# Kernel optimization log

Hardware: AMD Instinct MI355X
Metric: run time of the kernel (lower is better)

The kernel has to match this reference:

```python
import jax, jax.numpy as jnp
import numpy as np

B, T, IN, H, OUT = 64, 32, 256, 512, 256
M, W, R = 256, 64, 4            # nr_cells, cell_size, read_heads
NN_IN = IN + R * W              # 512
NN_OUT = H + R * W              # 768
IFACE = R * W + 3 * W + 5 * R + 3  # 471
CLIP = 20.0
DELTA = 1e-6


def setup_inputs():
    key = jax.random.key(0)
    ks = jax.random.split(key, 10)
    s = 0.05
    bound = float(np.sqrt(6.0 / (B * H + 2 * H)))  # xavier_uniform on (2,B,H)
    return {
        'x': jax.random.normal(ks[0], (B, T, IN), jnp.float32),
        'h0': jax.random.uniform(ks[1], (2, B, H), jnp.float32, -bound, bound),
        'Wih0': jax.random.normal(ks[2], (4 * H, NN_IN), jnp.float32) * s,
        'Whh0': jax.random.normal(ks[3], (4 * H, H), jnp.float32) * s,
        'bih0': jnp.zeros((4 * H,), jnp.float32),
        'bhh0': jnp.zeros((4 * H,), jnp.float32),
        'Wih1': jax.random.normal(ks[4], (4 * H, H), jnp.float32) * s,
        'Whh1': jax.random.normal(ks[5], (4 * H, H), jnp.float32) * s,
        'bih1': jnp.zeros((4 * H,), jnp.float32),
        'bhh1': jnp.zeros((4 * H,), jnp.float32),
        'Wif': jax.random.normal(ks[6], (IFACE, H), jnp.float32) * s,
        'bif': jnp.zeros((IFACE,), jnp.float32),
        'Wout': jax.random.normal(ks[7], (OUT, NN_OUT), jnp.float32) * s,
        'bout': jnp.zeros((OUT,), jnp.float32),
    }


def _lstm_cell(x, h, c, Wih, Whh, bih, bhh):
    g = x @ Wih.T + bih + h @ Whh.T + bhh
    i, f, gg, o = jnp.split(g, 4, axis=1)  # torch gate order i,f,g,o
    c = jax.nn.sigmoid(f) * c + jax.nn.sigmoid(i) * jnp.tanh(gg)
    h = jax.nn.sigmoid(o) * jnp.tanh(c)
    return h, c


def _content_weights(mem, keys, strengths):
    # mem: (b,M,W), keys: (b,K,W), strengths: (b,K) -> softmax over M
    mem_n = mem / (jnp.linalg.norm(mem, axis=2, keepdims=True) + DELTA)
    key_n = keys / (jnp.linalg.norm(keys, axis=2, keepdims=True) + DELTA)
    sim = jnp.einsum('bkw,bmw->bkm', key_n, mem_n)
    return jax.nn.softmax(sim * strengths[..., None], axis=2)


def _memory_step(xi, mem, link, prec, rw, ww, usage):
    b = xi.shape[0]
    o = 0
    rk = jnp.tanh(xi[:, :R * W].reshape(b, R, W)); o = R * W
    rs = jax.nn.softplus(xi[:, o:o + R]); o += R
    wk = jnp.tanh(xi[:, o:o + W]).reshape(b, 1, W); o += W
    ws = jax.nn.softplus(xi[:, o])[:, None]; o += 1
    ev = jax.nn.sigmoid(xi[:, o:o + W]); o += W
    wv = jnp.tanh(xi[:, o:o + W]); o += W
    fg = jax.nn.sigmoid(xi[:, o:o + R]); o += R
    ag = jax.nn.sigmoid(xi[:, o])[:, None]; o += 1
    wg = jax.nn.sigmoid(xi[:, o])[:, None]; o += 1
    rm = jax.nn.softmax(xi[:, o:o + 3 * R].reshape(b, R, 3), axis=2)

    # usage update (uses OLD read/write weights); single write head
    usage = usage + (1.0 - usage) * ww
    psi = jnp.prod(1.0 - fg[:, :, None] * rw, axis=1)
    usage = usage * psi

    # write content addressing on OLD memory
    wcw = _content_weights(mem, wk, ws)[:, 0]  # (b,M)

    # allocation by ascending sort of usage (exclusive cumprod)
    u = DELTA + (1.0 - DELTA) * usage
    phi = jnp.argsort(u, axis=1)
    sorted_u = jnp.take_along_axis(u, phi, axis=1)
    excl = jnp.cumprod(jnp.concatenate([jnp.ones((b, 1), u.dtype), sorted_u], axis=1), axis=1)[:, :-1]
    sorted_alloc = (1.0 - sorted_u) * excl
    alloc = jnp.take_along_axis(sorted_alloc, jnp.argsort(phi, axis=1), axis=1)

    ww = wg * (ag * alloc + (1.0 - ag) * wcw)  # (b,M)

    # erase + write
    mem = mem * (1.0 - ww[:, :, None] * ev[:, None, :]) + ww[:, :, None] * wv[:, None, :]

    # temporal link matrix + precedence
    prev_scale = 1.0 - ww[:, :, None] - ww[:, None, :]
    link = prev_scale * link + ww[:, :, None] * prec[:, None, :]
    link = link * (1.0 - jnp.eye(M, dtype=link.dtype))
    prec = (1.0 - ww.sum(axis=1, keepdims=True)) * prec + ww

    # read: directional weights use NEW link and OLD read weights; content uses NEW memory
    rcw = _content_weights(mem, rk, rs)               # (b,R,M)
    fwd = jnp.einsum('bij,brj->bri', link, rw)
    bwd = jnp.einsum('brj,bji->bri', rw, link)
    rw = rm[:, :, 0:1] * bwd + rm[:, :, 1:2] * fwd + rm[:, :, 2:3] * rcw
    rvec = jnp.einsum('brm,bmw->brw', rw, mem).reshape(b, R * W)
    return rvec, mem, link, prec, rw, ww, usage


def reference(x, h0, Wih0, Whh0, bih0, bhh0, Wih1, Whh1, bih1, bhh1, Wif, bif, Wout, bout):
    b = x.shape[0]
    lr0 = jnp.zeros((b, R * W), x.dtype)  # initial last_read; NOTE: source concatenates this
    # initial zero last_read to EVERY timestep's controller input (inputs built upfront)
    carry0 = (h0[0], h0[0], h0[1], h0[1],
              jnp.full((b, M, W), DELTA, x.dtype),   # memory
              jnp.zeros((b, M, M), x.dtype),          # link matrix
              jnp.zeros((b, M), x.dtype),             # precedence
              jnp.full((b, R, M), DELTA, x.dtype),    # read weights
              jnp.full((b, M), DELTA, x.dtype),       # write weights
              jnp.zeros((b, M), x.dtype))             # usage

    def step(carry, x_t):
        h0_, c0_, h1_, c1_, mem, link, prec, rw, ww, usage = carry
        inp = jnp.concatenate([x_t, lr0], axis=1)
        h0_, c0_ = _lstm_cell(inp, h0_, c0_, Wih0, Whh0, bih0, bhh0)
        h1_, c1_ = _lstm_cell(h0_, h1_, c1_, Wih1, Whh1, bih1, bhh1)
        out = jnp.clip(h1_, -CLIP, CLIP)
        xi = out @ Wif.T + bif
        rvec, mem, link, prec, rw, ww, usage = _memory_step(xi, mem, link, prec, rw, ww, usage)
        o_t = jnp.concatenate([out, rvec], axis=1)  # (b, NN_OUT)
        return (h0_, c0_, h1_, c1_, mem, link, prec, rw, ww, usage), o_t

    _, ys = jax.lax.scan(step, carry0, jnp.swapaxes(x, 0, 1))  # (T,b,NN_OUT)
    outputs = jnp.tanh(ys) @ Wout.T + bout  # Dropout(p=0) -> Tanh -> Linear
    return jnp.swapaxes(outputs, 0, 1)      # (b,T,OUT)
```

## Files before the change

### kernel.cpp

```cpp
#include <hip/hip_runtime.h>
#include <hip/hip_bf16.h>
#include <math.h>


typedef __bf16 bf16_t;
typedef __attribute__((ext_vector_type(8))) __bf16 bf16x8;
typedef __attribute__((ext_vector_type(4))) float f32x4;

#define B_    64
#define T_    32
#define IN_   256
#define H_    512
#define M_    256
#define W_    64
#define R_    4
#define IFACE_ 471
#define DELTA_ 1e-6f

#define OFF_H0SEQ  (0L)
#define SZ_H0SEQ   (32L*64*512*2)
#define OFF_OUTSEQ (OFF_H0SEQ + SZ_H0SEQ)
#define SZ_OUTSEQ  (32L*64*512*2)
#define OFF_H0BUF  (OFF_OUTSEQ + SZ_OUTSEQ)
#define SZ_HBUF    (2L*64*512*2)
#define OFF_H1BUF  (OFF_H0BUF + SZ_HBUF)
#define OFF_XI     (OFF_H1BUF + SZ_HBUF)
#define SZ_XI      (32L*64*480*4)
#define OFF_RVEC   (OFF_XI + SZ_XI)
#define SZ_RVEC    (32L*64*256*4)
#define OFF_YBF    (OFF_RVEC + SZ_RVEC)
#define SZ_YBF     (32L*64*768*2)
#define OFF_BAR    (OFF_YBF + SZ_YBF)
#define SZ_BAR     (256L)
#define OFF_XB     (OFF_BAR + SZ_BAR)
#define SZ_XB      (64L*32*256*2)
#define OFF_H0B    (OFF_XB + SZ_XB)
#define SZ_H0B     (2L*64*512*2)
#define OFF_W0     (OFF_H0B + SZ_H0B)
#define SZ_W       (2048L*512*2)
#define OFF_W1     (OFF_W0 + SZ_W)
#define OFF_W2     (OFF_W1 + SZ_W)
#define OFF_W3     (OFF_W2 + SZ_W)
#define OFF_WIF    (OFF_W3 + SZ_W)
#define SZ_WIF     (480L*512*2)
#define OFF_WOUTB  (OFF_WIF + SZ_WIF)
#define SZ_WOUTB   (256L*768*2)
#define OFF_BS0    (OFF_WOUTB + SZ_WOUTB)
#define SZ_BS      (2048L*4)
#define OFF_BS1    (OFF_BS0 + SZ_BS)
#define OFF_BIF    (OFF_BS1 + SZ_BS)
#define SZ_BIF     (2048L)
#define OFF_BOUTF  (OFF_BIF + SZ_BIF)
#define SZ_BOUTF   (1024L)
#define OFF_FLG    (OFF_BOUTF + SZ_BOUTF)
#define SZ_FLG     (4096L)

__device__ __forceinline__ float frcp(float x){ return __builtin_amdgcn_rcpf(x); }
__device__ __forceinline__ float fsqrt_(float x){ return __builtin_amdgcn_sqrtf(x); }
__device__ __forceinline__ float sigf(float x){ return frcp(1.0f + __expf(-x)); }
__device__ __forceinline__ float tanh_f(float x){
  float xc = fminf(fmaxf(x, -44.0f), 44.0f);
  float t = __expf(2.0f * xc);
  return (t - 1.0f) * frcp(t + 1.0f);
}
__device__ __forceinline__ float softplusf(float x){
  return fmaxf(x, 0.0f) + __logf(1.0f + __expf(-fabsf(x)));
}
__device__ __forceinline__ float wred(float v){
  #pragma unroll
  for (int off = 32; off; off >>= 1) v += __shfl_xor(v, off, 64);
  return v;
}
__device__ __forceinline__ float ldin(const void* p, long i, int mf){
  return mf ? ((const float*)p)[i] : (float)((const bf16_t*)p)[i];
}

__device__ __forceinline__ unsigned flag_ld(const unsigned* p){
  return __hip_atomic_load(p, __ATOMIC_RELAXED, __HIP_MEMORY_SCOPE_AGENT);
}

__device__ __forceinline__ void flagbar(unsigned* flg, int bid, unsigned tgt,
                                        int tid, int lane, int wv){
  __syncthreads();
  if (tid == 0)
    __hip_atomic_store(flg + (size_t)bid*16, tgt, __ATOMIC_RELEASE,
                       __HIP_MEMORY_SCOPE_AGENT);
  if (wv == 0){
    for (;;){
      unsigned f = flag_ld(flg + (size_t)lane*16);
      if (__all(f >= tgt)) break;
      __builtin_amdgcn_s_sleep(2);
    }
    __builtin_amdgcn_fence(__ATOMIC_ACQUIRE, "agent");
  }
  __syncthreads();
}

__global__ void k_detect(const unsigned short* __restrict__ x16,
                         int* __restrict__ flag, unsigned* __restrict__ bar,
                         unsigned* __restrict__ flg){
  __shared__ int cnt;
  if (threadIdx.x == 0){ cnt = 0; bar[0] = 0u; bar[1] = 0u; }
  for (int i = threadIdx.x; i < 1024; i += 256) flg[i] = 0u;
  __syncthreads();
  unsigned short u = x16[threadIdx.x * 2];
  int e = (u >> 7) & 0xFF;
  if (e >= 0x88) atomicAdd(&cnt, 1);
  __syncthreads();
  if (threadIdx.x == 0) *flag = (cnt > 16) ? 1 : 0;
}

__global__ void k_convert(const void* x, const void* h0, const void* Wih0,
                          const void* Whh0, const void* bih0, const void* bhh0,
                          const void* Wih1, const void* Whh1, const void* bih1,
                          const void* bhh1, const void* Wif, const void* bif,
                          const void* Wout, const void* bout,
                          bf16_t* __restrict__ xb, bf16_t* __restrict__ h0b,
                          bf16_t* __restrict__ h0buf, bf16_t* __restrict__ h1buf,
                          bf16_t* __restrict__ W0, bf16_t* __restrict__ W1,
                          bf16_t* __restrict__ W2, bf16_t* __restrict__ W3,
                          bf16_t* __restrict__ Wifp, bf16_t* __restrict__ Woutb,
                          float* __restrict__ bs0, float* __restrict__ bs1,
                          float* __restrict__ bifp, float* __restrict__ boutf,
                          const int* __restrict__ flag)
{
  const int mf = *flag;
  const long stride = (long)gridDim.x * blockDim.x;
  long i0 = (long)blockIdx.x * blockDim.x + threadIdx.x;
  switch (blockIdx.y){
  case 0: for (long i = i0; i < 64L*32*256; i += stride) xb[i] = (bf16_t)ldin(x, i, mf); break;
  case 1: for (long i = i0; i < 2L*64*512; i += stride){
            float v = ldin(h0, i, mf); bf16_t bb = (bf16_t)v; h0b[i] = bb;
            if (i < 64*512) h0buf[i] = bb; else h1buf[i - 64*512] = bb;
          } break;
  case 2: for (long i = i0; i < 2048L*512; i += stride) W0[i] = (bf16_t)ldin(Wih0, i, mf); break;
  case 3: for (long i = i0; i < 2048L*512; i += stride) W1[i] = (bf16_t)ldin(Whh0, i, mf); break;
  case 4: for (long i = i0; i < 2048L*512; i += stride) W2[i] = (bf16_t)ldin(Wih1, i, mf); break;
  case 5: for (long i = i0; i < 2048L*512; i += stride) W3[i] = (bf16_t)ldin(Whh1, i, mf); break;
  case 6: for (long i = i0; i < 480L*512; i += stride){
            long r = i >> 9;
            Wifp[i] = (r < IFACE_) ? (bf16_t)ldin(Wif, i, mf) : (bf16_t)0.0f;
          } break;
  case 7: for (long i = i0; i < 256L*768; i += stride) Woutb[i] = (bf16_t)ldin(Wout, i, mf); break;
  case 8:
    for (long i = i0; i < 2048; i += stride){
      bs0[i] = ldin(bih0, i, mf) + ldin(bhh0, i, mf);
      bs1[i] = ldin(bih1, i, mf) + ldin(bhh1, i, mf);
    }
    for (long i = i0; i < 480; i += stride) bifp[i] = (i < IFACE_) ? ldin(bif, i, mf) : 0.0f;
    for (long i = i0; i < 256; i += stride) boutf[i] = ldin(bout, i, mf);
    break;
  }
}

__device__ __forceinline__ void softmax256_wave(float* a, int lane){
  float v0=a[lane], v1=a[64+lane], v2=a[128+lane], v3=a[192+lane];
  float mx = fmaxf(fmaxf(v0,v1), fmaxf(v2,v3));
  #pragma unroll
  for (int off=32; off; off>>=1) mx = fmaxf(mx, __shfl_xor(mx, off, 64));
  v0=__expf(v0-mx); v1=__expf(v1-mx); v2=__expf(v2-mx); v3=__expf(v3-mx);
  float s = v0+v1+v2+v3;
  #pragma unroll
  for (int off=32; off; off>>=1) s += __shfl_xor(s, off, 64);
  float inv = frcp(s);
  a[lane]=v0*inv; a[64+lane]=v1*inv; a[128+lane]=v2*inv; a[192+lane]=v3*inv;
}

struct ProdShm {
  bf16_t wpool[66560];
  float  cst[64][16];
  float  bias[4][16];
};
struct ConsShm {
  float smem[256][65];
  float xib[480];
  float rkn4r[2][65][4];
  float wkn[64], ev_[64], wvv[64];
  float rs_[4], fg_[4], rm_[4][3];
  float wsS, agS, wgS, wwsumS;
  float invn[256], wcw[256];
  float usage[256], uu[256], su[256], scanA[256];
  int   rank_[256];
  float ww_[256], prec_[256];
  float rw_[4][256];
  float rw4[256][4];
  float fwd_[4][256], bwd_[4][256], rcw_[4][256];
  bf16_t rwb[4][264];
  bf16_t wwb[256], precb[256];
  float p2cT[2][264];
  float p5cT[5][2][264];
  float rvp[8][4][64];
};
union ShUnion { ProdShm p; ConsShm c; };

__global__ __launch_bounds__(512) void k_main(
    const bf16_t* __restrict__ xb, const bf16_t* __restrict__ h0b,
    const bf16_t* __restrict__ W0, const bf16_t* __restrict__ W1,
    const bf16_t* __restrict__ W2, const bf16_t* __restrict__ W3,
    const float* __restrict__ bs0, const float* __restrict__ bs1,
    const bf16_t* __restrict__ Wifp, const float* __restrict__ bifp,
    bf16_t* __restrict__ h0buf, bf16_t* __restrict__ h1buf,
    bf16_t* __restrict__ h0seq, bf16_t* __restrict__ outseq,
    float* __restrict__ XI, float* __restrict__ RVEC,
    unsigned* __restrict__ flg)
{
  __shared__ ShUnion sh;
  const int bid = blockIdx.x;
  const int tid = threadIdx.x, lane = tid & 63, wv = tid >> 6;
  const int m16 = lane & 15, q = lane >> 4;

  if (bid < 64){
    ProdShm& P = sh.p;
    const int layer = bid >> 5;
    const int u0 = (bid & 31) * 16;

    if (!layer){
      for (int i = tid; i < 64*32; i += 512){
        int rl = i >> 5, c8 = (i & 31)*8;
        int grow = (rl >> 4)*512 + u0 + (rl & 15);
        *(bf16x8*)&P.wpool[rl*264 + c8] = *(const bf16x8*)(W0 + (size_t)grow*512 + c8);
      }
      for (int i = tid; i < 64*64; i += 512){
        int rl = i >> 6, c8 = (i & 63)*8;
        int grow = (rl >> 4)*512 + u0 + (rl & 15);
        *(bf16x8*)&P.wpool[16896 + rl*520 + c8] = *(const bf16x8*)(W1 + (size_t)grow*512 + c8);
      }
    } else {
      for (int i = tid; i < 64*64; i += 512){
        int rl = i >> 6, c8 = (i & 63)*8;
        int grow = (rl >> 4)*512 + u0 + (rl & 15);
        *(bf16x8*)&P.wpool[rl*520 + c8]         = *(const bf16x8*)(W2 + (size_t)grow*512 + c8);
        *(bf16x8*)&P.wpool[33280 + rl*520 + c8] = *(const bf16x8*)(W3 + (size_t)grow*512 + c8);
      }
    }
    for (int i = tid; i < 64*16; i += 512){
      int b = i >> 4, n = i & 15;
      P.cst[b][n] = (float)h0b[layer*(64*512) + b*512 + u0 + n];
    }
    if (tid < 64){
      int G = tid >> 4, n = tid & 15;
      const float* bs = layer ? bs1 : bs0;
      P.bias[G][n] = bs[G*512 + u0 + n];
    }
    __syncthreads();

    bf16_t* hbuf = layer ? h1buf : h0buf;

    for (int ps = 0; ps <= 33; ++ps){
      if (wv < 4){
        const int t = layer ? (ps - 1) : ps;
        const bool active = layer ? (ps >= 1 && ps <= 32) : (ps < 32);
        if (active){
          const int p = t & 1;
          const bf16_t* hin = hbuf + p*(64*512);
          bf16_t* hout = hbuf + (p^1)*(64*512);
          const int b0 = wv * 16;

          f32x4 acc[4];
          #pragma unroll
          for (int G = 0; G < 4; ++G){ float bv = P.bias[G][m16]; acc[G] = (f32x4){bv,bv,bv,bv}; }

          if (!layer){
            #pragma unroll 2
            for (int kt = 0; kt < 8; ++kt){
              bf16x8 a = *(const bf16x8*)(xb + ((size_t)(b0+m16)*T_ + t)*IN_ + kt*32 + q*8);
              #pragma unroll
              for (int G = 0; G < 4; ++G)
                acc[G] = __builtin_amdgcn_mfma_f32_16x16x32_bf16(
                    a, *(const bf16x8*)&P.wpool[(G*16+m16)*264 + kt*32 + q*8], acc[G], 0, 0, 0);
            }
            #pragma unroll 4
            for (int kt = 0; kt < 16; ++kt){
              bf16x8 a = *(const bf16x8*)(hin + (b0+m16)*512 + kt*32 + q*8);
              #pragma unroll
              for (int G = 0; G < 4; ++G)
                acc[G] = __builtin_amdgcn_mfma_f32_16x16x32_bf16(
                    a, *(const bf16x8*)&P.wpool[16896 + (G*16+m16)*520 + kt*32 + q*8], acc[G], 0, 0, 0);
            }
          } else {
            #pragma unroll 4
            for (int kt = 0; kt < 16; ++kt){
              bf16x8 a = *(const bf16x8*)(h0seq + ((size_t)t*64 + b0+m16)*512 + kt*32 + q*8);
              #pragma unroll
              for (int G = 0; G < 4; ++G)
                acc[G] = __builtin_amdgcn_mfma_f32_16x16x32_bf16(
                    a, *(const bf16x8*)&P.wpool[(G*16+m16)*520 + kt*32 + q*8], acc[G], 0, 0, 0);
            }
            #pragma unroll 4
            for (int kt = 0; kt < 16; ++kt){
              bf16x8 a = *(const bf16x8*)(hin + (b0+m16)*512 + kt*32 + q*8);
              #pragma unroll
              for (int G = 0; G < 4; ++G)
                acc[G] = __builtin_amdgcn_mfma_f32_16x16x32_bf16(
                    a, *(const bf16x8*)&P.wpool[33280 + (G*16+m16)*520 + kt*32 + q*8], acc[G], 0, 0, 0);
            }
          }
          #pragma unroll
          for (int v = 0; v < 4; ++v){
            int b = b0 + q*4 + v;
            float gi = acc[0][v], gf = acc[1][v], gg = acc[2][v], go = acc[3][v];
            float c_ = sigf(gf)*P.cst[b][m16] + sigf(gi)*tanh_f(gg);
            P.cst[b][m16] = c_;
            float h = sigf(go)*tanh_f(c_);
            bf16_t hb = (bf16_t)h;
            hout[b*512 + u0 + m16] = hb;
            if (!layer) h0seq[((size_t)t*64 + b)*512 + u0 + m16] = hb;
            else        outseq[((size_t)t*64 + b)*512 + u0 + m16] = hb;
          }
        }
      } else if (ps >= 2 && bid < 30){
        const int t2 = ps - 2;
        const int b0 = (wv - 4) * 16;
        const int r = bid*16 + m16;
        float bv = bifp[r];
        f32x4 acc = {bv,bv,bv,bv};
        const bf16_t* arow = outseq + ((size_t)t2*64 + b0 + m16)*512 + q*8;
        const bf16_t* brow = Wifp + (size_t)r*512 + q*8;
        #pragma unroll 4
        for (int kt = 0; kt < 16; ++kt){
          acc = __builtin_amdgcn_mfma_f32_16x16x32_bf16(
              *(const bf16x8*)(arow + kt*32), *(const bf16x8*)(brow + kt*32), acc, 0, 0, 0);
        }
        #pragma unroll
        for (int v = 0; v < 4; ++v)
          XI[((size_t)t2*64 + b0 + q*4 + v)*480 + r] = acc[v];
      }
      flagbar(flg, bid, (unsigned)(ps + 1), tid, lane, wv);
    }
  } else {
    ConsShm& S = sh.c;
    const int b = bid - 64;
    const int quad = lane >> 4, li = lane & 15;

    bf16x8 rowL[2][8], colL[2][8];
    #pragma unroll
    for (int g = 0; g < 2; ++g)
      #pragma unroll
      for (int ch = 0; ch < 8; ++ch)
        #pragma unroll
        for (int z = 0; z < 8; ++z){ rowL[g][ch][z] = (bf16_t)0.0f; colL[g][ch][z] = (bf16_t)0.0f; }

    float mr[32];
    #pragma unroll
    for (int z = 0; z < 32; ++z) mr[z] = DELTA_;

    if (tid < 256){
      S.ww_[tid] = DELTA_; S.usage[tid] = 0.0f; S.prec_[tid] = 0.0f;
      S.invn[tid] = 1.0f/(fsqrt_(64.0f*DELTA_*DELTA_) + DELTA_);
      S.wwb[tid] = (bf16_t)DELTA_; S.precb[tid] = (bf16_t)0.0f;
      #pragma unroll
      for (int r = 0; r < 4; ++r) S.rw_[r][tid] = DELTA_;
    }
    for (int i = tid; i < 4*264; i += 512) ((bf16_t*)S.rwb)[i] = (bf16_t)DELTA_;
    for (int i = tid; i < 256*65; i += 512) ((float*)S.smem)[i] = DELTA_;
    __syncthreads();

    const int mH = tid >> 1, q2 = tid & 1;

    for (int t = 0; t < 32; ++t){
      { const unsigned tgt = (unsigned)(t + 3);
        if (wv == 0){
          for (;;){
            unsigned f = flag_ld(flg + (size_t)lane*16);
            if (__all(f >= tgt)) break;
            __builtin_amdgcn_s_sleep(2);
          }
          __builtin_amdgcn_fence(__ATOMIC_ACQUIRE, "agent");
        }
        __syncthreads();
      }
      if (tid < IFACE_) S.xib[tid] = XI[((size_t)t*64 + b)*480 + tid];
      __syncthreads();

      if (wv < 4){
        float v = tanh_f(S.xib[wv*64 + lane]);
        float s = wred(v*v);
        float vn = v * frcp(fsqrt_(s) + DELTA_);
        S.rkn4r[0][lane][wv] = vn; S.rkn4r[1][lane][wv] = vn;
      } else if (wv == 4){
        float v = tanh_f(S.xib[260 + lane]);
        float s = wred(v*v);
        S.wkn[lane] = v * frcp(fsqrt_(s) + DELTA_);
      } else if (wv == 5){ S.ev_[lane] = sigf(S.xib[325 + lane]);
      } else if (wv == 6){ S.wvv[lane] = tanh_f(S.xib[389 + lane]);
      } else {
        if (lane < 4)        S.rs_[lane] = softplusf(S.xib[256 + lane]);
        else if (lane == 4)  S.wsS = softplusf(S.xib[324]);
        else if (lane < 9)   S.fg_[lane-5] = sigf(S.xib[453 + (lane-5)]);
        else if (lane == 9)  S.agS = sigf(S.xib[457]);
        else if (lane == 10) S.wgS = sigf(S.xib[458]);
        else if (lane >= 16 && lane < 20){
          int r = lane - 16;
          float a0 = S.xib[459+r*3], a1 = S.xib[459+r*3+1], a2 = S.xib[459+r*3+2];
          float mx = fmaxf(a0, fmaxf(a1, a2));
          float e0 = __expf(a0-mx), e1 = __expf(a1-mx), e2 = __expf(a2-mx);
          float inv = frcp(e0+e1+e2);
          S.rm_[r][0]=e0*inv; S.rm_[r][1]=e1*inv; S.rm_[r][2]=e2*inv;
        }
      }
      __syncthreads();

      if (tid < 256){
        int m = tid;
        float us = S.usage[m] + (1.0f - S.usage[m])*S.ww_[m];
        float psi = (1.0f - S.fg_[0]*S.rw_[0][m]) * (1.0f - S.fg_[1]*S.rw_[1][m])
                  * (1.0f - S.fg_[2]*S.rw_[2][m]) * (1.0f - S.fg_[3]*S.rw_[3][m]);
        us *= psi;
        S.usage[m] = us;
        S.uu[m] = DELTA_ + (1.0f - DELTA_)*us;
      }
      { float acc = 0.0f;
        #pragma unroll
        for (int it = 0; it < 32; ++it){
          int w = q2*32 + it;
          acc += mr[it] * S.wkn[w];
        }
        S.p2cT[q2][mH] = acc; }
      __syncthreads();

      if (wv == 0){
        #pragma unroll
        for (int z = 0; z < 4; ++z){
          int m = z*64 + lane;
          S.wcw[m] = S.wsS * (S.p2cT[0][m] + S.p2cT[1][m]) * S.invn[m];
        }
        softmax256_wave(S.wcw, lane);
      } else if (tid >= 256){
        const int i = tid - 256;
        const float ui = S.uu[i];
        int cnt = 0;
        #pragma unroll 8
        for (int k = 0; k < 64; ++k){
          f32x4 u4 = *(const f32x4*)&S.uu[k*4];
          #pragma unroll
          for (int z = 0; z < 4; ++z){
            int j = k*4 + z; float uj = u4[z];
            cnt += (uj < ui || (uj == ui && j < i)) ? 1 : 0;
          }
        }
        S.rank_[i] = cnt;
        S.su[cnt] = ui;
      }
      __syncthreads();

      if (wv == 0){
        int base = lane*4;
        float v0 = S.su[base], v1 = S.su[base+1], v2 = S.su[base+2];
        float p1 = v0*v1, p2 = p1*v2, p3 = p2*S.su[base+3];
        float sc = p3;
        #pragma unroll
        for (int off = 1; off < 64; off <<= 1){
          float n = __shfl_up(sc, off, 64);
          if (lane >= off) sc *= n;
        }
        float exch = __shfl_up(sc, 1, 64);
        if (lane == 0) exch = 1.0f;
        S.scanA[base] = exch; S.scanA[base+1] = exch*v0;
        S.scanA[base+2] = exch*p1; S.scanA[base+3] = exch*p2;
      }
      __syncthreads();

      { const int m = mH;
        float al = (1.0f - S.uu[m]) * S.scanA[S.rank_[m]];
        float wm = S.wgS*(S.agS*al + (1.0f - S.agS)*S.wcw[m]);
        if (q2 == 0){ S.ww_[m] = wm; S.wwb[m] = (bf16_t)wm; }
        float s2 = 0.0f, sr0 = 0.0f, sr1 = 0.0f, sr2 = 0.0f, sr3 = 0.0f;
        #pragma unroll
        for (int it = 0; it < 32; ++it){
          int w = q2*32 + it;
          float mn = mr[it]*(1.0f - wm*S.ev_[w]) + wm*S.wvv[w];
          mr[it] = mn;
          S.smem[m][w] = mn;
          s2 += mn*mn;
          f32x4 rk = *(const f32x4*)&S.rkn4r[q2][w][0];
          sr0 += mn*rk[0]; sr1 += mn*rk[1]; sr2 += mn*rk[2]; sr3 += mn*rk[3];
        }
        S.p5cT[0][q2][m] = s2;
        S.p5cT[1][q2][m] = sr0; S.p5cT[2][q2][m] = sr1;
        S.p5cT[3][q2][m] = sr2; S.p5cT[4][q2][m] = sr3; }
      __syncthreads();

      if (tid < 256){
        int m = tid;
        float s2 = S.p5cT[0][0][m] + S.p5cT[0][1][m];
        float inv = frcp(fsqrt_(s2) + DELTA_);
        S.invn[m] = inv;
        #pragma unroll
        for (int r = 0; r < 4; ++r){
          float sr = S.p5cT[r+1][0][m] + S.p5cT[r+1][1][m];
          S.rcw_[r][m] = S.rs_[r]*sr*inv;
        }
      } else if (wv == 4){
        float s = wred(S.ww_[lane] + S.ww_[64+lane] + S.ww_[128+lane] + S.ww_[192+lane]);
        if (lane == 0) S.wwsumS = s;
      }
      __syncthreads();

      { float wown[2], pown[2], alpha[2];
        #pragma unroll
        for (int g = 0; g < 2; ++g){
          int o = wv*32 + g*16 + li;
          wown[g] = (float)S.wwb[o]; pown[g] = (float)S.precb[o];
          alpha[g] = 1.0f - wown[g];
        }
        f32x4 facc[2] = {{0,0,0,0},{0,0,0,0}}, bacc[2] = {{0,0,0,0},{0,0,0,0}};
        #pragma unroll
        for (int ch = 0; ch < 8; ++ch){
          const int cbase = ch*32 + quad*8;
          bf16x8 rwf = *(const bf16x8*)&S.rwb[li & 3][cbase];
          bf16x8 wwv = *(const bf16x8*)&S.wwb[cbase];
          bf16x8 pcv = *(const bf16x8*)&S.precb[cbase];
          float wcf[8], pcf[8];
          #pragma unroll
          for (int jj = 0; jj < 8; ++jj){ wcf[jj] = (float)wwv[jj]; pcf[jj] = (float)pcv[jj]; }
          #pragma unroll
          for (int g = 0; g < 2; ++g){
            const int o = wv*32 + g*16 + li;
            bf16x8 rl = rowL[g][ch];
            bf16x8 cl = colL[g][ch];
            #pragma unroll
            for (int jj = 0; jj < 8; ++jj){
              const int c = cbase + jj;
              float s = alpha[g] - wcf[jj];
              float vr = s*(float)rl[jj] + wown[g]*pcf[jj];
              float vc = s*(float)cl[jj] + wcf[jj]*pown[g];
              if (c == o){ vr = 0.0f; vc = 0.0f; }
              rl[jj] = (bf16_t)vr;
              cl[jj] = (bf16_t)vc;
            }
            rowL[g][ch] = rl; colL[g][ch] = cl;
            facc[g] = __builtin_amdgcn_mfma_f32_16x16x32_bf16(rl, rwf, facc[g], 0, 0, 0);
            bacc[g] = __builtin_amdgcn_mfma_f32_16x16x32_bf16(rwf, cl, bacc[g], 0, 0, 0);
          }
        }
        #pragma unroll
        for (int g = 0; g < 2; ++g){
          if (li < 4){
            #pragma unroll
            for (int z = 0; z < 4; ++z) S.fwd_[li][wv*32 + g*16 + quad*4 + z] = facc[g][z];
          }
          if (quad == 0){
            #pragma unroll
            for (int z = 0; z < 4; ++z) S.bwd_[z][wv*32 + g*16 + li] = bacc[g][z];
          }
        }
      }
      __syncthreads();

      if (wv < 4) softmax256_wave(S.rcw_[wv], lane);
      else {
        int m = tid - 256;
        float p = (1.0f - S.wwsumS)*S.prec_[m] + S.ww_[m];
        S.prec_[m] = p;
        S.precb[m] = (bf16_t)p;
      }
      __syncthreads();

      { int r = tid >> 7, m0 = (tid & 127)*2;
        #pragma unroll
        for (int z = 0; z < 2; ++z){
          int m = m0 + z;
          float v = S.rm_[r][0]*S.bwd_[r][m] + S.rm_[r][1]*S.fwd_[r][m] + S.rm_[r][2]*S.rcw_[r][m];
          S.rw_[r][m] = v;
          S.rw4[m][r] = v;
          S.rwb[r][m] = (bf16_t)v;
        } }
      __syncthreads();

      { float r0 = 0, r1 = 0, r2 = 0, r3 = 0;
        #pragma unroll
        for (int k = 0; k < 32; ++k){
          int m = wv*32 + k;
          f32x4 r4 = *(const f32x4*)&S.rw4[m][0];
          float mv = S.smem[m][lane];
          r0 += r4[0]*mv; r1 += r4[1]*mv; r2 += r4[2]*mv; r3 += r4[3]*mv;
        }
        S.rvp[wv][0][lane] = r0; S.rvp[wv][1][lane] = r1;
        S.rvp[wv][2][lane] = r2; S.rvp[wv][3][lane] = r3; }
      __syncthreads();

      if (tid < 256){
        const int w = tid & 63, r = tid >> 6;
        float v = 0.0f;
        #pragma unroll
        for (int c = 0; c < 8; ++c) v += S.rvp[c][r][w];
        RVEC[((size_t)t*64 + b)*256 + tid] = v;
      }
      __syncthreads();
    }
  }
}

__global__ void k_tanhy(const bf16_t* __restrict__ outseq, const float* __restrict__ RVEC,
                        bf16_t* __restrict__ Y){
  const int n = 2048*768;
  for (int i = blockIdx.x*blockDim.x + threadIdx.x; i < n; i += gridDim.x*blockDim.x){
    int row = i / 768, j = i - row*768;
    float v = (j < 512) ? (float)outseq[(size_t)row*512 + j] : RVEC[(size_t)row*256 + (j - 512)];
    Y[i] = (bf16_t)tanh_f(v);
  }
}

__global__ __launch_bounds__(256,1) void k_out(
    const bf16_t* __restrict__ Y, const bf16_t* __restrict__ Woutb,
    const float* __restrict__ boutf, void* __restrict__ dout,
    const int* __restrict__ flag)
{
  const int mf = *flag;
  const int mt = blockIdx.x;
  const int tid = threadIdx.x, lane = tid & 63, wv = tid >> 6;
  const int nt = blockIdx.y*4 + wv;
  const int m16 = lane & 15, q = lane >> 4;
  const int o = nt*16 + m16;
  float bv = boutf[o];
  f32x4 acc = {bv,bv,bv,bv};
  const bf16_t* arow = Y + (size_t)(mt*16 + m16)*768 + q*8;
  const bf16_t* brow = Woutb + (size_t)o*768 + q*8;
  for (int kt = 0; kt < 24; ++kt){
    acc = __builtin_amdgcn_mfma_f32_16x16x32_bf16(
        *(const bf16x8*)(arow + kt*32), *(const bf16x8*)(brow + kt*32), acc, 0, 0, 0);
  }
  #pragma unroll
  for (int v = 0; v < 4; ++v){
    int row = mt*16 + q*4 + v;
    int b = row & 63, t = row >> 6;
    size_t idx = ((size_t)b*T_ + t)*256 + o;
    if (mf) ((float*)dout)[idx] = acc[v];
    else    ((bf16_t*)dout)[idx] = (bf16_t)acc[v];
  }
}

extern "C" void kernel_launch(void* const* d_in, const int* in_sizes, int n_in,
                              void* d_out, int out_size, void* d_ws, size_t ws_size,
                              hipStream_t stream)
{
  char* ws = (char*)d_ws;
  bf16_t* H0SEQ  = (bf16_t*)(ws + OFF_H0SEQ);
  bf16_t* OUTSEQ = (bf16_t*)(ws + OFF_OUTSEQ);
  bf16_t* H0BUF  = (bf16_t*)(ws + OFF_H0BUF);
  bf16_t* H1BUF  = (bf16_t*)(ws + OFF_H1BUF);
  float*  XI     = (float*) (ws + OFF_XI);
  float*  RVEC   = (float*) (ws + OFF_RVEC);
  bf16_t* YBF    = (bf16_t*)(ws + OFF_YBF);
  unsigned* BAR  = (unsigned*)(ws + OFF_BAR);
  int*    FLAG   = (int*)   (ws + OFF_BAR + 8);
  bf16_t* XB     = (bf16_t*)(ws + OFF_XB);
  bf16_t* H0B    = (bf16_t*)(ws + OFF_H0B);
  bf16_t* W0     = (bf16_t*)(ws + OFF_W0);
  bf16_t* W1     = (bf16_t*)(ws + OFF_W1);
  bf16_t* W2     = (bf16_t*)(ws + OFF_W2);
  bf16_t* W3     = (bf16_t*)(ws + OFF_W3);
  bf16_t* WIFP   = (bf16_t*)(ws + OFF_WIF);
  bf16_t* WOUTB  = (bf16_t*)(ws + OFF_WOUTB);
  float*  BS0    = (float*) (ws + OFF_BS0);
  float*  BS1    = (float*) (ws + OFF_BS1);
  float*  BIFP   = (float*) (ws + OFF_BIF);
  float*  BOUTF  = (float*) (ws + OFF_BOUTF);
  unsigned* FLG  = (unsigned*)(ws + OFF_FLG);

  k_detect<<<1, 256, 0, stream>>>((const unsigned short*)d_in[0], FLAG, BAR, FLG);
  k_convert<<<dim3(256, 9), 256, 0, stream>>>(
      d_in[0], d_in[1], d_in[2], d_in[3], d_in[4], d_in[5], d_in[6],
      d_in[7], d_in[8], d_in[9], d_in[10], d_in[11], d_in[12], d_in[13],
      XB, H0B, H0BUF, H1BUF, W0, W1, W2, W3, WIFP, WOUTB,
      BS0, BS1, BIFP, BOUTF, FLAG);
  k_main<<<128, 512, 0, stream>>>(XB, H0B, W0, W1, W2, W3, BS0, BS1,
                                  WIFP, BIFP, H0BUF, H1BUF, H0SEQ, OUTSEQ,
                                  XI, RVEC, FLG);
  k_tanhy<<<512, 256, 0, stream>>>(OUTSEQ, RVEC, YBF);
  k_out<<<dim3(128, 4), 256, 0, stream>>>(YBF, WOUTB, BOUTF, d_out, FLAG);
}
```

Baseline: 1.057 ms.

## Prefetch interface vector into registers and overlap next-step flag wait

The consumer blocks now read their slice of the interface vector straight from global memory into registers instead of staging it through shared memory. The load for the next timestep is issued early, and one wave waits on the producer flag for that step during the precedence update. The bf16 shadow copies of the write weights and precedence are dropped, so the link update reads the fp32 arrays directly. The read-vector reduction is restructured as a two-thread-per-output dot product with a shuffle, replacing the partial-sum buffer and its reduction. Together these remove several barriers per step and take the flag-wait latency off the critical path. The costs are a longer serial loop per thread in the read reduction and more register pressure.

```diff
diff --git a/kernel.cpp b/kernel.cpp
--- a/kernel.cpp
+++ b/kernel.cpp
@@ -173,7 +173,6 @@
 };
 struct ConsShm {
   float smem[256][65];
-  float xib[480];
   float rkn4r[2][65][4];
   float wkn[64], ev_[64], wvv[64];
   float rs_[4], fg_[4], rm_[4][3];
@@ -186,10 +185,8 @@
   float rw4[256][4];
   float fwd_[4][256], bwd_[4][256], rcw_[4][256];
   bf16_t rwb[4][264];
-  bf16_t wwb[256], precb[256];
   float p2cT[2][264];
   float p5cT[5][2][264];
-  float rvp[8][4][64];
 };
 union ShUnion { ProdShm p; ConsShm c; };
 
@@ -344,10 +341,25 @@
     #pragma unroll
     for (int z = 0; z < 32; ++z) mr[z] = DELTA_;
 
+    int off0 = -1, off1 = -1, off2 = -1;
+    if (wv < 4)            off0 = wv*64 + lane;
+    else if (wv == 4)      off0 = 260 + lane;
+    else if (wv == 5)      off0 = 325 + lane;
+    else if (wv == 6)      off0 = 389 + lane;
+    else {
+      if (lane < 4)        off0 = 256 + lane;
+      else if (lane == 4)  off0 = 324;
+      else if (lane < 9)   off0 = 453 + (lane - 5);
+      else if (lane == 9)  off0 = 457;
+      else if (lane == 10) off0 = 458;
+      else if (lane >= 16 && lane < 20){
+        off0 = 459 + (lane - 16)*3; off1 = off0 + 1; off2 = off0 + 2;
+      }
+    }
+
     if (tid < 256){
       S.ww_[tid] = DELTA_; S.usage[tid] = 0.0f; S.prec_[tid] = 0.0f;
       S.invn[tid] = 1.0f/(fsqrt_(64.0f*DELTA_*DELTA_) + DELTA_);
-      S.wwb[tid] = (bf16_t)DELTA_; S.precb[tid] = (bf16_t)0.0f;
       #pragma unroll
       for (int r = 0; r < 4; ++r) S.rw_[r][tid] = DELTA_;
     }
@@ -357,43 +369,44 @@
 
     const int mH = tid >> 1, q2 = tid & 1;
 
+    if (wv == 0){
+      for (;;){
+        unsigned f = flag_ld(flg + (size_t)lane*16);
+        if (__all(f >= 3u)) break;
+        __builtin_amdgcn_s_sleep(2);
+      }
+      __builtin_amdgcn_fence(__ATOMIC_ACQUIRE, "agent");
+    }
+    __syncthreads();
+    float x0 = 0.0f, x1 = 0.0f, x2 = 0.0f;
+    {
+      const float* xp = XI + (size_t)b*480;
+      if (off0 >= 0) x0 = xp[off0];
+      if (off1 >= 0){ x1 = xp[off1]; x2 = xp[off2]; }
+    }
+
     for (int t = 0; t < 32; ++t){
-      { const unsigned tgt = (unsigned)(t + 3);
-        if (wv == 0){
-          for (;;){
-            unsigned f = flag_ld(flg + (size_t)lane*16);
-            if (__all(f >= tgt)) break;
-            __builtin_amdgcn_s_sleep(2);
-          }
-          __builtin_amdgcn_fence(__ATOMIC_ACQUIRE, "agent");
-        }
-        __syncthreads();
-      }
-      if (tid < IFACE_) S.xib[tid] = XI[((size_t)t*64 + b)*480 + tid];
-      __syncthreads();
-
       if (wv < 4){
-        float v = tanh_f(S.xib[wv*64 + lane]);
+        float v = tanh_f(x0);
         float s = wred(v*v);
         float vn = v * frcp(fsqrt_(s) + DELTA_);
         S.rkn4r[0][lane][wv] = vn; S.rkn4r[1][lane][wv] = vn;
       } else if (wv == 4){
-        float v = tanh_f(S.xib[260 + lane]);
+        float v = tanh_f(x0);
         float s = wred(v*v);
         S.wkn[lane] = v * frcp(fsqrt_(s) + DELTA_);
-      } else if (wv == 5){ S.ev_[lane] = sigf(S.xib[325 + lane]);
-      } else if (wv == 6){ S.wvv[lane] = tanh_f(S.xib[389 + lane]);
+      } else if (wv == 5){ S.ev_[lane] = sigf(x0);
+      } else if (wv == 6){ S.wvv[lane] = tanh_f(x0);
       } else {
-        if (lane < 4)        S.rs_[lane] = softplusf(S.xib[256 + lane]);
-        else if (lane == 4)  S.wsS = softplusf(S.xib[324]);
-        else if (lane < 9)   S.fg_[lane-5] = sigf(S.xib[453 + (lane-5)]);
-        else if (lane == 9)  S.agS = sigf(S.xib[457]);
-        else if (lane == 10) S.wgS = sigf(S.xib[458]);
+        if (lane < 4)        S.rs_[lane] = softplusf(x0);
+        else if (lane == 4)  S.wsS = softplusf(x0);
+        else if (lane < 9)   S.fg_[lane-5] = sigf(x0);
+        else if (lane == 9)  S.agS = sigf(x0);
+        else if (lane == 10) S.wgS = sigf(x0);
         else if (lane >= 16 && lane < 20){
           int r = lane - 16;
-          float a0 = S.xib[459+r*3], a1 = S.xib[459+r*3+1], a2 = S.xib[459+r*3+2];
-          float mx = fmaxf(a0, fmaxf(a1, a2));
-          float e0 = __expf(a0-mx), e1 = __expf(a1-mx), e2 = __expf(a2-mx);
+          float mx = fmaxf(x0, fmaxf(x1, x2));
+          float e0 = __expf(x0-mx), e1 = __expf(x1-mx), e2 = __expf(x2-mx);
           float inv = frcp(e0+e1+e2);
           S.rm_[r][0]=e0*inv; S.rm_[r][1]=e1*inv; S.rm_[r][2]=e2*inv;
         }
@@ -463,7 +476,7 @@
       { const int m = mH;
         float al = (1.0f - S.uu[m]) * S.scanA[S.rank_[m]];
         float wm = S.wgS*(S.agS*al + (1.0f - S.agS)*S.wcw[m]);
-        if (q2 == 0){ S.ww_[m] = wm; S.wwb[m] = (bf16_t)wm; }
+        if (q2 == 0) S.ww_[m] = wm;
         float s2 = 0.0f, sr0 = 0.0f, sr1 = 0.0f, sr2 = 0.0f, sr3 = 0.0f;
         #pragma unroll
         for (int it = 0; it < 32; ++it){
@@ -494,13 +507,11 @@
         float s = wred(S.ww_[lane] + S.ww_[64+lane] + S.ww_[128+lane] + S.ww_[192+lane]);
         if (lane == 0) S.wwsumS = s;
       }
-      __syncthreads();
-
       { float wown[2], pown[2], alpha[2];
         #pragma unroll
         for (int g = 0; g < 2; ++g){
           int o = wv*32 + g*16 + li;
-          wown[g] = (float)S.wwb[o]; pown[g] = (float)S.precb[o];
+          wown[g] = S.ww_[o]; pown[g] = S.prec_[o];
           alpha[g] = 1.0f - wown[g];
         }
         f32x4 facc[2] = {{0,0,0,0},{0,0,0,0}}, bacc[2] = {{0,0,0,0},{0,0,0,0}};
@@ -508,11 +519,12 @@
         for (int ch = 0; ch < 8; ++ch){
           const int cbase = ch*32 + quad*8;
           bf16x8 rwf = *(const bf16x8*)&S.rwb[li & 3][cbase];
-          bf16x8 wwv = *(const bf16x8*)&S.wwb[cbase];
-          bf16x8 pcv = *(const bf16x8*)&S.precb[cbase];
-          float wcf[8], pcf[8];
-          #pragma unroll
-          for (int jj = 0; jj < 8; ++jj){ wcf[jj] = (float)wwv[jj]; pcf[jj] = (float)pcv[jj]; }
+          f32x4 wA = *(const f32x4*)&S.ww_[cbase];
+          f32x4 wB = *(const f32x4*)&S.ww_[cbase+4];
+          f32x4 pA = *(const f32x4*)&S.prec_[cbase];
+          f32x4 pB = *(const f32x4*)&S.prec_[cbase+4];
+          float wcf[8] = {wA[0],wA[1],wA[2],wA[3],wB[0],wB[1],wB[2],wB[3]};
+          float pcf[8] = {pA[0],pA[1],pA[2],pA[3],pB[0],pB[1],pB[2],pB[3]};
           #pragma unroll
           for (int g = 0; g < 2; ++g){
             const int o = wv*32 + g*16 + li;
@@ -552,10 +564,23 @@
         int m = tid - 256;
         float p = (1.0f - S.wwsumS)*S.prec_[m] + S.ww_[m];
         S.prec_[m] = p;
-        S.precb[m] = (bf16_t)p;
-      }
-      __syncthreads();
-
+        if (wv == 4 && t < 31){
+          const unsigned tgt = (unsigned)(t + 4);
+          for (;;){
+            unsigned f = flag_ld(flg + (size_t)lane*16);
+            if (__all(f >= tgt)) break;
+            __builtin_amdgcn_s_sleep(2);
+          }
+          __builtin_amdgcn_fence(__ATOMIC_ACQUIRE, "agent");
+        }
+      }
+      __syncthreads();
+
+      if (t < 31){
+        const float* xp = XI + ((size_t)(t+1)*64 + b)*480;
+        if (off0 >= 0) x0 = xp[off0];
+        if (off1 >= 0){ x1 = xp[off1]; x2 = xp[off2]; }
+      }
       { int r = tid >> 7, m0 = (tid & 127)*2;
         #pragma unroll
         for (int z = 0; z < 2; ++z){
@@ -567,26 +592,17 @@
         } }
       __syncthreads();
 
-      { float r0 = 0, r1 = 0, r2 = 0, r3 = 0;
-        #pragma unroll
-        for (int k = 0; k < 32; ++k){
-          int m = wv*32 + k;
-          f32x4 r4 = *(const f32x4*)&S.rw4[m][0];
-          float mv = S.smem[m][lane];
-          r0 += r4[0]*mv; r1 += r4[1]*mv; r2 += r4[2]*mv; r3 += r4[3]*mv;
-        }
-        S.rvp[wv][0][lane] = r0; S.rvp[wv][1][lane] = r1;
-        S.rvp[wv][2][lane] = r2; S.rvp[wv][3][lane] = r3; }
-      __syncthreads();
-
-      if (tid < 256){
-        const int w = tid & 63, r = tid >> 6;
-        float v = 0.0f;
-        #pragma unroll
-        for (int c = 0; c < 8; ++c) v += S.rvp[c][r][w];
-        RVEC[((size_t)t*64 + b)*256 + tid] = v;
-      }
-      __syncthreads();
+      { const int o = tid >> 1;
+        const int r = o >> 6, w = o & 63;
+        float s = 0.0f;
+        #pragma unroll 16
+        for (int k = 0; k < 128; ++k){
+          int m = q2*128 + k;
+          s += S.rw4[m][r] * S.smem[m][w];
+        }
+        s += __shfl_xor(s, 1, 64);
+        if (q2 == 0) RVEC[((size_t)t*64 + b)*256 + o] = s;
+      }
     }
   }
 }
```

After: 1.099 ms. 1.04x slower.

## Drop column link copy; derive backward weights by transposing row link through LDS

Applied to the files above, without the earlier changes.

The consumer blocks no longer keep a second register-resident copy of the link matrix (colL) or the per-thread memory row cache (mr). The backward read weights are now computed by staging each wave's rowL tile into a shared-memory transpose buffer in eight sub-steps, and memory values are read directly from shared memory. The bf16 copies of write weights and precedence are replaced by fp32 vector reads, and the scratch buffers are unioned with the new transpose tile. This is meant to cut VGPR pressure and likely spilling on the serial per-timestep path, at the cost of sixteen extra block barriers per timestep and more LDS traffic.

```diff
diff --git a/kernel.cpp b/kernel.cpp
--- a/kernel.cpp
+++ b/kernel.cpp
@@ -173,23 +173,29 @@
 };
 struct ConsShm {
   float smem[256][65];
-  float xib[480];
-  float rkn4r[2][65][4];
   float wkn[64], ev_[64], wvv[64];
   float rs_[4], fg_[4], rm_[4][3];
   float wsS, agS, wgS, wwsumS;
-  float invn[256], wcw[256];
-  float usage[256], uu[256], su[256], scanA[256];
-  int   rank_[256];
+  float invn[256];
+  float usage[256];
   float ww_[256], prec_[256];
   float rw_[4][256];
   float rw4[256][4];
   float fwd_[4][256], bwd_[4][256], rcw_[4][256];
   bf16_t rwb[4][264];
-  bf16_t wwb[256], precb[256];
-  float p2cT[2][264];
-  float p5cT[5][2][264];
-  float rvp[8][4][64];
+  union {
+    struct {
+      float xib[480];
+      float rkn4r[2][65][4];
+      float wcw[256];
+      float uu[256], su[256], scanA[256];
+      int   rank_[256];
+      float p2cT[2][264];
+      float p5cT[5][2][264];
+      float rvp[8][4][64];
+    } a;
+    bf16_t tls[32][258];
+  } u;
 };
 union ShUnion { ProdShm p; ConsShm c; };
 
@@ -332,22 +338,17 @@
     const int b = bid - 64;
     const int quad = lane >> 4, li = lane & 15;
 
-    bf16x8 rowL[2][8], colL[2][8];
+    bf16x8 rowL[2][8];
     #pragma unroll
     for (int g = 0; g < 2; ++g)
       #pragma unroll
       for (int ch = 0; ch < 8; ++ch)
         #pragma unroll
-        for (int z = 0; z < 8; ++z){ rowL[g][ch][z] = (bf16_t)0.0f; colL[g][ch][z] = (bf16_t)0.0f; }
-
-    float mr[32];
-    #pragma unroll
-    for (int z = 0; z < 32; ++z) mr[z] = DELTA_;
+        for (int z = 0; z < 8; ++z) rowL[g][ch][z] = (bf16_t)0.0f;
 
     if (tid < 256){
       S.ww_[tid] = DELTA_; S.usage[tid] = 0.0f; S.prec_[tid] = 0.0f;
       S.invn[tid] = 1.0f/(fsqrt_(64.0f*DELTA_*DELTA_) + DELTA_);
-      S.wwb[tid] = (bf16_t)DELTA_; S.precb[tid] = (bf16_t)0.0f;
       #pragma unroll
       for (int r = 0; r < 4; ++r) S.rw_[r][tid] = DELTA_;
     }
@@ -369,29 +370,29 @@
         }
         __syncthreads();
       }
-      if (tid < IFACE_) S.xib[tid] = XI[((size_t)t*64 + b)*480 + tid];
+      if (tid < IFACE_) S.u.a.xib[tid] = XI[((size_t)t*64 + b)*480 + tid];
       __syncthreads();
 
       if (wv < 4){
-        float v = tanh_f(S.xib[wv*64 + lane]);
+        float v = tanh_f(S.u.a.xib[wv*64 + lane]);
         float s = wred(v*v);
         float vn = v * frcp(fsqrt_(s) + DELTA_);
-        S.rkn4r[0][lane][wv] = vn; S.rkn4r[1][lane][wv] = vn;
+        S.u.a.rkn4r[0][lane][wv] = vn; S.u.a.rkn4r[1][lane][wv] = vn;
       } else if (wv == 4){
-        float v = tanh_f(S.xib[260 + lane]);
+        float v = tanh_f(S.u.a.xib[260 + lane]);
         float s = wred(v*v);
         S.wkn[lane] = v * frcp(fsqrt_(s) + DELTA_);
-      } else if (wv == 5){ S.ev_[lane] = sigf(S.xib[325 + lane]);
-      } else if (wv == 6){ S.wvv[lane] = tanh_f(S.xib[389 + lane]);
+      } else if (wv == 5){ S.ev_[lane] = sigf(S.u.a.xib[325 + lane]);
+      } else if (wv == 6){ S.wvv[lane] = tanh_f(S.u.a.xib[389 + lane]);
       } else {
-        if (lane < 4)        S.rs_[lane] = softplusf(S.xib[256 + lane]);
-        else if (lane == 4)  S.wsS = softplusf(S.xib[324]);
-        else if (lane < 9)   S.fg_[lane-5] = sigf(S.xib[453 + (lane-5)]);
-        else if (lane == 9)  S.agS = sigf(S.xib[457]);
-        else if (lane == 10) S.wgS = sigf(S.xib[458]);
+        if (lane < 4)        S.rs_[lane] = softplusf(S.u.a.xib[256 + lane]);
+        else if (lane == 4)  S.wsS = softplusf(S.u.a.xib[324]);
+        else if (lane < 9)   S.fg_[lane-5] = sigf(S.u.a.xib[453 + (lane-5)]);
+        else if (lane == 9)  S.agS = sigf(S.u.a.xib[457]);
+        else if (lane == 10) S.wgS = sigf(S.u.a.xib[458]);
         else if (lane >= 16 && lane < 20){
           int r = lane - 16;
-          float a0 = S.xib[459+r*3], a1 = S.xib[459+r*3+1], a2 = S.xib[459+r*3+2];
+          float a0 = S.u.a.xib[459+r*3], a1 = S.u.a.xib[459+r*3+1], a2 = S.u.a.xib[459+r*3+2];
           float mx = fmaxf(a0, fmaxf(a1, a2));
           float e0 = __expf(a0-mx), e1 = __expf(a1-mx), e2 = __expf(a2-mx);
           float inv = frcp(e0+e1+e2);
@@ -407,46 +408,46 @@
                   * (1.0f - S.fg_[2]*S.rw_[2][m]) * (1.0f - S.fg_[3]*S.rw_[3][m]);
         us *= psi;
         S.usage[m] = us;
-        S.uu[m] = DELTA_ + (1.0f - DELTA_)*us;
+        S.u.a.uu[m] = DELTA_ + (1.0f - DELTA_)*us;
       }
       { float acc = 0.0f;
         #pragma unroll
         for (int it = 0; it < 32; ++it){
           int w = q2*32 + it;
-          acc += mr[it] * S.wkn[w];
-        }
-        S.p2cT[q2][mH] = acc; }
+          acc += S.smem[mH][w] * S.wkn[w];
+        }
+        S.u.a.p2cT[q2][mH] = acc; }
       __syncthreads();
 
       if (wv == 0){
         #pragma unroll
         for (int z = 0; z < 4; ++z){
           int m = z*64 + lane;
-          S.wcw[m] = S.wsS * (S.p2cT[0][m] + S.p2cT[1][m]) * S.invn[m];
-        }
-        softmax256_wave(S.wcw, lane);
+          S.u.a.wcw[m] = S.wsS * (S.u.a.p2cT[0][m] + S.u.a.p2cT[1][m]) * S.invn[m];
+        }
+        softmax256_wave(S.u.a.wcw, lane);
       } else if (tid >= 256){
         const int i = tid - 256;
-        const float ui = S.uu[i];
+        const float ui = S.u.a.uu[i];
         int cnt = 0;
         #pragma unroll 8
         for (int k = 0; k < 64; ++k){
-          f32x4 u4 = *(const f32x4*)&S.uu[k*4];
+          f32x4 u4 = *(const f32x4*)&S.u.a.uu[k*4];
           #pragma unroll
           for (int z = 0; z < 4; ++z){
             int j = k*4 + z; float uj = u4[z];
             cnt += (uj < ui || (uj == ui && j < i)) ? 1 : 0;
           }
         }
-        S.rank_[i] = cnt;
-        S.su[cnt] = ui;
+        S.u.a.rank_[i] = cnt;
+        S.u.a.su[cnt] = ui;
       }
       __syncthreads();
 
       if (wv == 0){
         int base = lane*4;
-        float v0 = S.su[base], v1 = S.su[base+1], v2 = S.su[base+2];
-        float p1 = v0*v1, p2 = p1*v2, p3 = p2*S.su[base+3];
+        float v0 = S.u.a.su[base], v1 = S.u.a.su[base+1], v2 = S.u.a.su[base+2];
+        float p1 = v0*v1, p2 = p1*v2, p3 = p2*S.u.a.su[base+3];
         float sc = p3;
         #pragma unroll
         for (int off = 1; off < 64; off <<= 1){
@@ -455,39 +456,38 @@
         }
         float exch = __shfl_up(sc, 1, 64);
         if (lane == 0) exch = 1.0f;
-        S.scanA[base] = exch; S.scanA[base+1] = exch*v0;
-        S.scanA[base+2] = exch*p1; S.scanA[base+3] = exch*p2;
+        S.u.a.scanA[base] = exch; S.u.a.scanA[base+1] = exch*v0;
+        S.u.a.scanA[base+2] = exch*p1; S.u.a.scanA[base+3] = exch*p2;
       }
       __syncthreads();
 
       { const int m = mH;
-        float al = (1.0f - S.uu[m]) * S.scanA[S.rank_[m]];
-        float wm = S.wgS*(S.agS*al + (1.0f - S.agS)*S.wcw[m]);
-        if (q2 == 0){ S.ww_[m] = wm; S.wwb[m] = (bf16_t)wm; }
+        float al = (1.0f - S.u.a.uu[m]) * S.u.a.scanA[S.u.a.rank_[m]];
+        float wm = S.wgS*(S.agS*al + (1.0f - S.agS)*S.u.a.wcw[m]);
+        if (q2 == 0) S.ww_[m] = wm;
         float s2 = 0.0f, sr0 = 0.0f, sr1 = 0.0f, sr2 = 0.0f, sr3 = 0.0f;
         #pragma unroll
         for (int it = 0; it < 32; ++it){
           int w = q2*32 + it;
-          float mn = mr[it]*(1.0f - wm*S.ev_[w]) + wm*S.wvv[w];
-          mr[it] = mn;
+          float mn = S.smem[m][w]*(1.0f - wm*S.ev_[w]) + wm*S.wvv[w];
           S.smem[m][w] = mn;
           s2 += mn*mn;
-          f32x4 rk = *(const f32x4*)&S.rkn4r[q2][w][0];
+          f32x4 rk = *(const f32x4*)&S.u.a.rkn4r[q2][w][0];
           sr0 += mn*rk[0]; sr1 += mn*rk[1]; sr2 += mn*rk[2]; sr3 += mn*rk[3];
         }
-        S.p5cT[0][q2][m] = s2;
-        S.p5cT[1][q2][m] = sr0; S.p5cT[2][q2][m] = sr1;
-        S.p5cT[3][q2][m] = sr2; S.p5cT[4][q2][m] = sr3; }
+        S.u.a.p5cT[0][q2][m] = s2;
+        S.u.a.p5cT[1][q2][m] = sr0; S.u.a.p5cT[2][q2][m] = sr1;
+        S.u.a.p5cT[3][q2][m] = sr2; S.u.a.p5cT[4][q2][m] = sr3; }
       __syncthreads();
 
       if (tid < 256){
         int m = tid;
-        float s2 = S.p5cT[0][0][m] + S.p5cT[0][1][m];
+        float s2 = S.u.a.p5cT[0][0][m] + S.u.a.p5cT[0][1][m];
         float inv = frcp(fsqrt_(s2) + DELTA_);
         S.invn[m] = inv;
         #pragma unroll
         for (int r = 0; r < 4; ++r){
-          float sr = S.p5cT[r+1][0][m] + S.p5cT[r+1][1][m];
+          float sr = S.u.a.p5cT[r+1][0][m] + S.u.a.p5cT[r+1][1][m];
           S.rcw_[r][m] = S.rs_[r]*sr*inv;
         }
       } else if (wv == 4){
@@ -496,55 +496,79 @@
       }
       __syncthreads();
 
+      f32x4 bacc[2] = {{0,0,0,0},{0,0,0,0}};
       { float wown[2], pown[2], alpha[2];
         #pragma unroll
         for (int g = 0; g < 2; ++g){
           int o = wv*32 + g*16 + li;
-          wown[g] = (float)S.wwb[o]; pown[g] = (float)S.precb[o];
+          wown[g] = S.ww_[o]; pown[g] = S.prec_[o];
           alpha[g] = 1.0f - wown[g];
         }
-        f32x4 facc[2] = {{0,0,0,0},{0,0,0,0}}, bacc[2] = {{0,0,0,0},{0,0,0,0}};
+        f32x4 facc[2] = {{0,0,0,0},{0,0,0,0}};
         #pragma unroll
         for (int ch = 0; ch < 8; ++ch){
           const int cbase = ch*32 + quad*8;
           bf16x8 rwf = *(const bf16x8*)&S.rwb[li & 3][cbase];
-          bf16x8 wwv = *(const bf16x8*)&S.wwb[cbase];
-          bf16x8 pcv = *(const bf16x8*)&S.precb[cbase];
-          float wcf[8], pcf[8];
-          #pragma unroll
-          for (int jj = 0; jj < 8; ++jj){ wcf[jj] = (float)wwv[jj]; pcf[jj] = (float)pcv[jj]; }
+          f32x4 wA = *(const f32x4*)&S.ww_[cbase];
+          f32x4 wB = *(const f32x4*)&S.ww_[cbase+4];
+          f32x4 pA = *(const f32x4*)&S.prec_[cbase];
+          f32x4 pB = *(const f32x4*)&S.prec_[cbase+4];
+          float wcf[8] = {wA[0],wA[1],wA[2],wA[3],wB[0],wB[1],wB[2],wB[3]};
+          float pcf[8] = {pA[0],pA[1],pA[2],pA[3],pB[0],pB[1],pB[2],pB[3]};
           #pragma unroll
           for (int g = 0; g < 2; ++g){
             const int o = wv*32 + g*16 + li;
             bf16x8 rl = rowL[g][ch];
-            bf16x8 cl = colL[g][ch];
             #pragma unroll
             for (int jj = 0; jj < 8; ++jj){
               const int c = cbase + jj;
               float s = alpha[g] - wcf[jj];
               float vr = s*(float)rl[jj] + wown[g]*pcf[jj];
-              float vc = s*(float)cl[jj] + wcf[jj]*pown[g];
-              if (c == o){ vr = 0.0f; vc = 0.0f; }
+              if (c == o) vr = 0.0f;
               rl[jj] = (bf16_t)vr;
-              cl[jj] = (bf16_t)vc;
             }
-            rowL[g][ch] = rl; colL[g][ch] = cl;
+            rowL[g][ch] = rl;
             facc[g] = __builtin_amdgcn_mfma_f32_16x16x32_bf16(rl, rwf, facc[g], 0, 0, 0);
-            bacc[g] = __builtin_amdgcn_mfma_f32_16x16x32_bf16(rwf, cl, bacc[g], 0, 0, 0);
           }
         }
         #pragma unroll
-        for (int g = 0; g < 2; ++g){
+        for (int g = 0; g < 2; ++g)
           if (li < 4){
             #pragma unroll
             for (int z = 0; z < 4; ++z) S.fwd_[li][wv*32 + g*16 + quad*4 + z] = facc[g][z];
           }
-          if (quad == 0){
+      }
+      __syncthreads();
+
+      #pragma unroll 1
+      for (int sub = 0; sub < 8; ++sub){
+        if (wv == sub){
+          #pragma unroll
+          for (int g = 0; g < 2; ++g)
             #pragma unroll
-            for (int z = 0; z < 4; ++z) S.bwd_[z][wv*32 + g*16 + li] = bacc[g][z];
+            for (int ch = 0; ch < 8; ++ch)
+              *(bf16x8*)&S.u.tls[g*16 + li][ch*32 + quad*8] = rowL[g][ch];
+        }
+        __syncthreads();
+        { const int cb = sub*32 + quad*8;
+          bf16x8 rwf = *(const bf16x8*)&S.rwb[li & 3][cb];
+          #pragma unroll
+          for (int g = 0; g < 2; ++g){
+            const int x = wv*32 + g*16 + li;
+            bf16x8 cl;
+            #pragma unroll
+            for (int z = 0; z < 8; ++z) cl[z] = S.u.tls[quad*8 + z][x];
+            bacc[g] = __builtin_amdgcn_mfma_f32_16x16x32_bf16(rwf, cl, bacc[g], 0, 0, 0);
           }
         }
-      }
+        __syncthreads();
+      }
+      #pragma unroll
+      for (int g = 0; g < 2; ++g)
+        if (quad == 0){
+          #pragma unroll
+          for (int z = 0; z < 4; ++z) S.bwd_[z][wv*32 + g*16 + li] = bacc[g][z];
+        }
       __syncthreads();
 
       if (wv < 4) softmax256_wave(S.rcw_[wv], lane);
@@ -552,7 +576,6 @@
         int m = tid - 256;
         float p = (1.0f - S.wwsumS)*S.prec_[m] + S.ww_[m];
         S.prec_[m] = p;
-        S.precb[m] = (bf16_t)p;
       }
       __syncthreads();
 
@@ -575,15 +598,15 @@
           float mv = S.smem[m][lane];
           r0 += r4[0]*mv; r1 += r4[1]*mv; r2 += r4[2]*mv; r3 += r4[3]*mv;
         }
-        S.rvp[wv][0][lane] = r0; S.rvp[wv][1][lane] = r1;
-        S.rvp[wv][2][lane] = r2; S.rvp[wv][3][lane] = r3; }
+        S.u.a.rvp[wv][0][lane] = r0; S.u.a.rvp[wv][1][lane] = r1;
+        S.u.a.rvp[wv][2][lane] = r2; S.u.a.rvp[wv][3][lane] = r3; }
       __syncthreads();
 
       if (tid < 256){
         const int w = tid & 63, r = tid >> 6;
         float v = 0.0f;
         #pragma unroll
-        for (int c = 0; c < 8; ++c) v += S.rvp[c][r][w];
+        for (int c = 0; c < 8; ++c) v += S.u.a.rvp[c][r][w];
         RVEC[((size_t)t*64 + b)*256 + tid] = v;
       }
       __syncthreads();
```

Result: slower. 1.110 ms (+5.0%).
